# Kernel optimization log

Measured on AMD Instinct MI355X. Metric: run time of the kernel, lower is better.

The kernel has to match this reference:

```python
import jax, jax.numpy as jnp
import numpy as np

D_MODEL = 1024
NUM_HEADS = 16
HEAD_DIM = D_MODEL // NUM_HEADS
HIDDEN = 4096
EPS = 1e-5


def setup_inputs() -> dict:
    key = jax.random.key(0)
    ks = jax.random.split(key, 10)
    s = 0.02
    return {
        "x": jax.random.normal(ks[0], (2, 2048, D_MODEL), dtype=jnp.float32),
        # attention projection weights stored as (in, out): y = x @ W
        "wq": jax.random.normal(ks[1], (D_MODEL, D_MODEL), dtype=jnp.float32) * s,
        "wk": jax.random.normal(ks[2], (D_MODEL, D_MODEL), dtype=jnp.float32) * s,
        "wv": jax.random.normal(ks[3], (D_MODEL, D_MODEL), dtype=jnp.float32) * s,
        "wo": jax.random.normal(ks[4], (D_MODEL, D_MODEL), dtype=jnp.float32) * s,
        # FFN
        "w1": jax.random.normal(ks[5], (D_MODEL, HIDDEN), dtype=jnp.float32) * s,
        "b1": jnp.zeros((HIDDEN,), dtype=jnp.float32),
        "w2": jax.random.normal(ks[6], (HIDDEN, D_MODEL), dtype=jnp.float32) * s,
        "b2": jnp.zeros((D_MODEL,), dtype=jnp.float32),
        # LayerNorms
        "g1": jnp.ones((D_MODEL,), dtype=jnp.float32),
        "be1": jnp.zeros((D_MODEL,), dtype=jnp.float32),
        "g2": jnp.ones((D_MODEL,), dtype=jnp.float32),
        "be2": jnp.zeros((D_MODEL,), dtype=jnp.float32),
    }


def _layernorm(x, g, b):
    mu = jnp.mean(x, axis=-1, keepdims=True)
    var = jnp.mean(jnp.square(x - mu), axis=-1, keepdims=True)
    return (x - mu) * jax.lax.rsqrt(var + EPS) * g + b


def _attention(x, wq, wk, wv, wo):
    B, S, D = x.shape
    q = (x @ wq).reshape(B, S, NUM_HEADS, HEAD_DIM)
    k = (x @ wk).reshape(B, S, NUM_HEADS, HEAD_DIM)
    v = (x @ wv).reshape(B, S, NUM_HEADS, HEAD_DIM)
    scores = jnp.einsum("bqhd,bkhd->bhqk", q, k) / jnp.sqrt(
        jnp.float32(HEAD_DIM)
    )
    causal = jnp.tril(jnp.ones((S, S), dtype=bool))
    scores = jnp.where(causal, scores, -jnp.inf)
    probs = jax.nn.softmax(scores, axis=-1)
    out = jnp.einsum("bhqk,bkhd->bqhd", probs, v).reshape(B, S, D)
    return out @ wo


def _ffn(x, w1, b1, w2, b2):
    return jax.nn.relu(x @ w1 + b1) @ w2 + b2


def reference(x, wq, wk, wv, wo, w1, b1, w2, b2, g1, be1, g2, be2):
    x = x + _attention(_layernorm(x, g1, be1), wq, wk, wv, wo)
    x = x + _ffn(_layernorm(x, g2, be2), w1, b1, w2, b2)
    return x
```

## Files before the change

### kernel.cpp

```cpp
#include <hip/hip_runtime.h>
#include <stdint.h>

typedef unsigned short bf16u;
typedef __attribute__((ext_vector_type(8))) __bf16 bf16x8;
typedef __attribute__((ext_vector_type(4))) float f32x4;
typedef __attribute__((ext_vector_type(4))) unsigned short u16x4;
typedef __attribute__((ext_vector_type(8))) unsigned short u16x8;

typedef __attribute__((address_space(1))) void gvoid_t;
typedef __attribute__((address_space(3))) void lvoid_t;

#define SEQ 2048
#define DM 1024
#define MN22 4194304
#define SCL 0.18033688f

__device__ __forceinline__ bf16u f2bf(float f) {
  union { float f; uint32_t u; } v; v.f = f;
  uint32_t u = v.u + 0x7fffu + ((v.u >> 16) & 1u);
  return (bf16u)(u >> 16);
}

__device__ __forceinline__ bf16u f2bf_hw(float f) {
  union { __bf16 h; bf16u u; } v; v.h = (__bf16)f; return v.u;
}

__device__ __forceinline__ float bf2f(bf16u b) {
  union { uint32_t u; float f; } v; v.u = (uint32_t)b << 16; return v.f;
}

__device__ __forceinline__ float exp2_hw(float x) {
  return __builtin_amdgcn_exp2f(x);
}

__device__ __forceinline__ void async_copy16(const bf16u* g, const bf16u* l) {
  __builtin_amdgcn_global_load_lds((gvoid_t*)(uintptr_t)g,
                                   (lvoid_t*)(uint32_t)(uintptr_t)l,
                                   16, 0, 0);
}

#define VM_WAIT(n) asm volatile("s_waitcnt vmcnt(" #n ")" ::: "memory")
#define LGKM0()    asm volatile("s_waitcnt lgkmcnt(0)" ::: "memory")
#define BARRIER()  asm volatile("s_barrier" ::: "memory")

__global__ __launch_bounds__(256) void ln_kernel(const float* __restrict__ x,
                                                 const float* __restrict__ g,
                                                 const float* __restrict__ be,
                                                 bf16u* __restrict__ out) {
  const int row = blockIdx.x;
  const int t = threadIdx.x;
  const float4 v = ((const float4*)(x + (size_t)row * DM))[t];
  float s  = v.x + v.y + v.z + v.w;
  float ss = v.x * v.x + v.y * v.y + v.z * v.z + v.w * v.w;
#pragma unroll
  for (int m = 1; m < 64; m <<= 1) {
    s  += __shfl_xor(s, m, 64);
    ss += __shfl_xor(ss, m, 64);
  }
  __shared__ float red[2][4];
  const int wv = t >> 6, ln = t & 63;
  if (ln == 0) { red[0][wv] = s; red[1][wv] = ss; }
  __syncthreads();
  s  = red[0][0] + red[0][1] + red[0][2] + red[0][3];
  ss = red[1][0] + red[1][1] + red[1][2] + red[1][3];
  const float mu = s * (1.0f / DM);
  const float var = ss * (1.0f / DM) - mu * mu;
  const float rstd = rsqrtf(var + 1e-5f);
  const float4 gg = ((const float4*)g)[t];
  const float4 bb = ((const float4*)be)[t];
  u16x4 o;
  o[0] = f2bf((v.x - mu) * rstd * gg.x + bb.x);
  o[1] = f2bf((v.y - mu) * rstd * gg.y + bb.y);
  o[2] = f2bf((v.z - mu) * rstd * gg.z + bb.z);
  o[3] = f2bf((v.w - mu) * rstd * gg.w + bb.w);
  *(u16x4*)(out + (size_t)row * DM + t * 4) = o;
}

__global__ __launch_bounds__(256) void prep_kernel(
    const float* __restrict__ x, const float* __restrict__ g,
    const float* __restrict__ be, bf16u* __restrict__ lnout,
    const float* __restrict__ wq, const float* __restrict__ wk,
    const float* __restrict__ wv_, const float* __restrict__ wo,
    bf16u* __restrict__ wqkv_t,
    const float* __restrict__ w1, bf16u* __restrict__ w1_t,
    const float* __restrict__ w2, bf16u* __restrict__ w2_t) {
  const int bid = blockIdx.x;
  const int t = threadIdx.x;
  if (bid < 4096) {
    const int row = bid;
    const float4 v = ((const float4*)(x + (size_t)row * DM))[t];
    float s  = v.x + v.y + v.z + v.w;
    float ss = v.x * v.x + v.y * v.y + v.z * v.z + v.w * v.w;
#pragma unroll
    for (int m = 1; m < 64; m <<= 1) {
      s  += __shfl_xor(s, m, 64);
      ss += __shfl_xor(ss, m, 64);
    }
    __shared__ float red[2][4];
    const int wv = t >> 6, ln = t & 63;
    if (ln == 0) { red[0][wv] = s; red[1][wv] = ss; }
    __syncthreads();
    s  = red[0][0] + red[0][1] + red[0][2] + red[0][3];
    ss = red[1][0] + red[1][1] + red[1][2] + red[1][3];
    const float mu = s * (1.0f / DM);
    const float var = ss * (1.0f / DM) - mu * mu;
    const float rstd = rsqrtf(var + 1e-5f);
    const float4 gg = ((const float4*)g)[t];
    const float4 bb = ((const float4*)be)[t];
    u16x4 o;
    o[0] = f2bf((v.x - mu) * rstd * gg.x + bb.x);
    o[1] = f2bf((v.y - mu) * rstd * gg.y + bb.y);
    o[2] = f2bf((v.z - mu) * rstd * gg.z + bb.z);
    o[3] = f2bf((v.w - mu) * rstd * gg.w + bb.w);
    *(u16x4*)(lnout + (size_t)row * DM + t * 4) = o;
    return;
  }
  __shared__ float tile[32][33];
  const int tx = t & 31, ty = t >> 5;
  const float* in; bf16u* o; int R, C, c0, r0;
  if (bid < 8192) {
    const int idx = bid - 4096;
    const int mat = idx >> 10, rem = idx & 1023;
    const float* srcs[4] = {wq, wk, wv_, wo};
    in = srcs[mat]; o = wqkv_t + (size_t)mat * 1024 * 1024;
    R = 1024; C = 1024;
    c0 = (rem & 31) * 32; r0 = (rem >> 5) * 32;
  } else if (bid < 12288) {
    const int idx = bid - 8192;
    in = w1; o = w1_t; R = 1024; C = 4096;
    c0 = (idx & 127) * 32; r0 = (idx >> 7) * 32;
  } else {
    const int idx = bid - 12288;
    in = w2; o = w2_t; R = 4096; C = 1024;
    c0 = (idx & 31) * 32; r0 = (idx >> 5) * 32;
  }
#pragma unroll
  for (int i = 0; i < 4; ++i)
    tile[ty + i * 8][tx] = in[(size_t)(r0 + ty + i * 8) * C + c0 + tx];
  __syncthreads();
#pragma unroll
  for (int i = 0; i < 4; ++i)
    o[(size_t)(c0 + ty + i * 8) * R + r0 + tx] = f2bf(tile[tx][ty + i * 8]);
}

__global__ __launch_bounds__(256) void reduce3(const bf16u* __restrict__ p01,
                                               const bf16u* __restrict__ p2,
                                               const float* __restrict__ bias,
                                               float* __restrict__ out) {
  const size_t i8 = ((size_t)blockIdx.x * 256 + threadIdx.x) * 8;
  const int col0 = (int)(i8 & 1023);
  const u16x8 a = *(const u16x8*)(p01 + i8);
  const u16x8 b = *(const u16x8*)(p01 + MN22 + i8);
  const u16x8 c = *(const u16x8*)(p2 + i8);
  const float4 o0 = *(const float4*)(out + i8);
  const float4 o1 = *(const float4*)(out + i8 + 4);
  const float4 b0 = *(const float4*)(bias + col0);
  const float4 b1 = *(const float4*)(bias + col0 + 4);
  float r[8];
#pragma unroll
  for (int j = 0; j < 8; ++j) r[j] = bf2f(a[j]) + bf2f(b[j]) + bf2f(c[j]);
  float4 w0, w1;
  w0.x = o0.x + r[0] + b0.x; w0.y = o0.y + r[1] + b0.y;
  w0.z = o0.z + r[2] + b0.z; w0.w = o0.w + r[3] + b0.w;
  w1.x = o1.x + r[4] + b1.x; w1.y = o1.y + r[5] + b1.y;
  w1.z = o1.z + r[6] + b1.z; w1.w = o1.w + r[7] + b1.w;
  *(float4*)(out + i8) = w0;
  *(float4*)(out + i8 + 4) = w1;
}

__global__ __launch_bounds__(256, 2) void gemm256(
    const bf16u* __restrict__ A, const bf16u* __restrict__ Bt,
    int M, int N, int K,
    const float* __restrict__ bias, bf16u* __restrict__ outB,
    bf16u* __restrict__ vt, int mode) {
  __shared__ bf16u sh[2][16384];
  const int t = threadIdx.x;
  const int ln = t & 63;
  const int wv = t >> 6;
  const int col16 = ln & 15, quad = ln >> 4;
  const int wm = wv >> 1, wn = wv & 1;

  const int nsplit = (mode == 6) ? 3 : 1;
  const int nbx = N >> 7;
  const int nwg = nbx * (M >> 7) * nsplit;
  const int cpx = nwg >> 3;
  const int bid = blockIdx.x;
  const int swz = (bid & 7) * cpx + (bid >> 3);
  const int tile = swz / nsplit, split = swz - tile * nsplit;
  const int m0 = (tile / nbx) << 7, n0 = (tile % nbx) << 7;
  const int tsteps = K >> 6;
  const int kbeg = (split * tsteps) / nsplit;
  const int nt = ((split + 1) * tsteps) / nsplit - kbeg;
  const size_t koff = (size_t)kbeg << 6;

  const bf16u* gsrc[4][2];
  int doff[4][2];
#pragma unroll
  for (int j = 0; j < 2; ++j) {
    const int c = t + (j << 8);
    const int lr = c >> 3, slot = (c & 7) ^ (lr & 7);
    const int rq = (lr & 31) + ((lr >> 5) << 6);
    gsrc[0][j] = A  + (size_t)(m0 + rq) * K + koff + slot * 8;
    gsrc[3][j] = A  + (size_t)(m0 + rq + 32) * K + koff + slot * 8;
    gsrc[1][j] = Bt + (size_t)(n0 + rq) * K + koff + slot * 8;
    gsrc[2][j] = Bt + (size_t)(n0 + rq + 32) * K + koff + slot * 8;
    doff[0][j] = c * 8;
    doff[3][j] = 4096 + c * 8;
    doff[1][j] = 8192 + c * 8;
    doff[2][j] = 12288 + c * 8;
  }

  int aoffs[4][2], boffs[4][2];
#pragma unroll
  for (int i = 0; i < 4; ++i)
#pragma unroll
    for (int kc = 0; kc < 2; ++kc) {
      const int ra = wm * 64 + i * 16 + col16;
      const int la = ((ra >> 5) & 1) * 4096 + (((ra & 31) + ((ra >> 6) << 5)) << 6);
      aoffs[i][kc] = la + (((kc << 2) + quad) ^ (ra & 7)) * 8;
      const int rb = wn * 64 + i * 16 + col16;
      const int lb = ((rb >> 5) & 1) * 4096 + (((rb & 31) + ((rb >> 6) << 5)) << 6);
      boffs[i][kc] = 8192 + lb + (((kc << 2) + quad) ^ (rb & 7)) * 8;
    }

  f32x4 acc[4][4] = {};
  bf16x8 Af[2][2], Bf[4][2];

  auto stage = [&](int s, int b) {
#pragma unroll
    for (int j = 0; j < 2; ++j) {
      async_copy16(gsrc[s][j], &sh[b][doff[s][j]]);
      gsrc[s][j] += 64;
    }
  };
  auto readA = [&](int b, int mh) {
#pragma unroll
    for (int i = 0; i < 2; ++i)
#pragma unroll
      for (int kc = 0; kc < 2; ++kc)
        Af[i][kc] = *(const bf16x8*)(&sh[b][aoffs[mh * 2 + i][kc]]);
  };
  auto readB = [&](int b, int nh) {
#pragma unroll
    for (int i = 0; i < 2; ++i)
#pragma unroll
      for (int kc = 0; kc < 2; ++kc)
        Bf[nh * 2 + i][kc] = *(const bf16x8*)(&sh[b][boffs[nh * 2 + i][kc]]);
  };
  auto mfmaQ = [&](int mh, int nh) {
#pragma unroll
    for (int kc = 0; kc < 2; ++kc)
#pragma unroll
      for (int mi = 0; mi < 2; ++mi)
#pragma unroll
        for (int nl = 0; nl < 2; ++nl)
          acc[mh * 2 + mi][nh * 2 + nl] = __builtin_amdgcn_mfma_f32_16x16x32_bf16(
              Af[mi][kc], Bf[nh * 2 + nl][kc], acc[mh * 2 + mi][nh * 2 + nl], 0, 0, 0);
  };

  stage(0, 0); stage(1, 0); stage(2, 0); stage(3, 0);
  VM_WAIT(4);
  BARRIER();

  int bsel = 0;
  for (int kt = 0; kt < nt - 1; ++kt, bsel ^= 1) {
    const int bn = bsel ^ 1;
    readA(bsel, 0); readB(bsel, 0);
    stage(0, bn);
    BARRIER(); LGKM0();
    __builtin_amdgcn_s_setprio(1); mfmaQ(0, 0); __builtin_amdgcn_s_setprio(0);
    VM_WAIT(4); BARRIER();
    readB(bsel, 1);
    stage(1, bn);
    BARRIER(); LGKM0();
    __builtin_amdgcn_s_setprio(1); mfmaQ(0, 1); __builtin_amdgcn_s_setprio(0);
    VM_WAIT(4); BARRIER();
    readA(bsel, 1);
    stage(2, bn);
    BARRIER(); LGKM0();
    __builtin_amdgcn_s_setprio(1); mfmaQ(1, 0); __builtin_amdgcn_s_setprio(0);
    BARRIER();
    stage(3, bn);
    __builtin_amdgcn_s_setprio(1); mfmaQ(1, 1); __builtin_amdgcn_s_setprio(0);
    VM_WAIT(4); BARRIER();
  }
  readA(bsel, 0); readB(bsel, 0);
  BARRIER(); LGKM0();
  __builtin_amdgcn_s_setprio(1); mfmaQ(0, 0); __builtin_amdgcn_s_setprio(0);
  VM_WAIT(2); BARRIER();
  readB(bsel, 1);
  BARRIER(); LGKM0();
  __builtin_amdgcn_s_setprio(1); mfmaQ(0, 1); __builtin_amdgcn_s_setprio(0);
  VM_WAIT(0); BARRIER();
  readA(bsel, 1);
  LGKM0();
  __builtin_amdgcn_s_setprio(1); mfmaQ(1, 0); mfmaQ(1, 1); __builtin_amdgcn_s_setprio(0);

  if (mode == 6) {
    bf16u* pb = (split < 2) ? outB + (size_t)split * MN22 : vt;
#pragma unroll
    for (int mi = 0; mi < 4; ++mi) {
#pragma unroll
      for (int n = 0; n < 4; ++n) {
        const int col = n0 + wn * 64 + n * 16 + col16;
#pragma unroll
        for (int r = 0; r < 4; ++r) {
          const int row = m0 + wm * 64 + mi * 16 + quad * 4 + r;
          pb[(size_t)row * N + col] = f2bf(acc[mi][n][r]);
        }
      }
    }
    return;
  }
  if (mode == 5 && n0 >= 2048) {
#pragma unroll
    for (int mi = 0; mi < 4; ++mi) {
#pragma unroll
      for (int n = 0; n < 4; ++n) {
        const int col = n0 + wn * 64 + n * 16 + col16;
        const int hh = (col - 2048) >> 6, d = (col - 2048) & 63;
        const int row_base = m0 + wm * 64 + mi * 16 + quad * 4;
        const int bb = row_base >> 11, s = row_base & 2047;
        u16x4 o;
#pragma unroll
        for (int r = 0; r < 4; ++r) o[r] = f2bf(acc[mi][n][r]);
        *(u16x4*)(vt + (size_t)((bb * 16 + hh) * 64 + d) * SEQ + s) = o;
      }
    }
    return;
  }
  const float qscale = (mode == 5 && n0 < 1024) ? SCL : 1.0f;
  float bv[4];
  if (mode == 1) {
#pragma unroll
    for (int n = 0; n < 4; ++n) bv[n] = bias[n0 + wn * 64 + n * 16 + col16];
  }
#pragma unroll
  for (int mi = 0; mi < 4; ++mi) {
#pragma unroll
    for (int n = 0; n < 4; ++n) {
      const int col = n0 + wn * 64 + n * 16 + col16;
#pragma unroll
      for (int r = 0; r < 4; ++r) {
        const int row = m0 + wm * 64 + mi * 16 + quad * 4 + r;
        float v = acc[mi][n][r];
        if (mode == 1) v = fmaxf(v + bv[n], 0.0f);
        outB[(size_t)row * N + col] = f2bf(v * qscale);
      }
    }
  }
}

__global__ __launch_bounds__(256, 3) void gemm_bt64(
    const bf16u* __restrict__ A, const bf16u* __restrict__ Bt,
    int M, int N, int K,
    const float* __restrict__ bias, const float* __restrict__ resid,
    bf16u* __restrict__ outB, float* __restrict__ outF, int mode) {
  __shared__ bf16u As0[64 * 64], As1[64 * 64];
  __shared__ bf16u Bs0[128 * 64], Bs1[128 * 64];
  const int t = threadIdx.x;
  const int ln = t & 63;
  const int wv = t >> 6;
  const int col16 = ln & 15, quad = ln >> 4;

  const int nbx = gridDim.x;
  const int nwg = nbx * gridDim.y;
  const int cpx = nwg >> 3;
  const int flat = blockIdx.y * nbx + blockIdx.x;
  const int swz = (flat & 7) * cpx + (flat >> 3);
  const int m0 = (swz / nbx) * 64, n0 = (swz % nbx) * 128;

  const bf16u* gA[2];
  const bf16u* gB[4];
#pragma unroll
  for (int j = 0; j < 2; ++j) {
    const int c = t + 256 * j, row = c >> 3, slot = (c & 7) ^ (row & 7);
    gA[j] = A + (size_t)(m0 + row) * K + slot * 8;
  }
#pragma unroll
  for (int j = 0; j < 4; ++j) {
    const int c = t + 256 * j, row = c >> 3, slot = (c & 7) ^ (row & 7);
    gB[j] = Bt + (size_t)(n0 + row) * K + slot * 8;
  }

  f32x4 acc[4][2] = {};

  auto stage = [&](bf16u* dA, bf16u* dB) {
#pragma unroll
    for (int j = 0; j < 2; ++j) {
      async_copy16(gA[j], dA + (size_t)(t + 256 * j) * 8);
      gA[j] += 64;
    }
#pragma unroll
    for (int j = 0; j < 4; ++j) {
      async_copy16(gB[j], dB + (size_t)(t + 256 * j) * 8);
      gB[j] += 64;
    }
  };
  auto compute = [&](const bf16u* sA, const bf16u* sB) {
    bf16x8 af[4][2], bfv[2][2];
#pragma unroll
    for (int mi = 0; mi < 4; ++mi) {
      const int row = mi * 16 + col16;
#pragma unroll
      for (int kc = 0; kc < 2; ++kc)
        af[mi][kc] = *(const bf16x8*)(sA + row * 64 + (((kc << 2) + quad) ^ (row & 7)) * 8);
    }
#pragma unroll
    for (int ni = 0; ni < 2; ++ni) {
      const int row = wv * 32 + ni * 16 + col16;
#pragma unroll
      for (int kc = 0; kc < 2; ++kc)
        bfv[ni][kc] = *(const bf16x8*)(sB + row * 64 + (((kc << 2) + quad) ^ (row & 7)) * 8);
    }
#pragma unroll
    for (int kc = 0; kc < 2; ++kc)
#pragma unroll
      for (int mi = 0; mi < 4; ++mi)
#pragma unroll
        for (int ni = 0; ni < 2; ++ni)
          acc[mi][ni] = __builtin_amdgcn_mfma_f32_16x16x32_bf16(af[mi][kc], bfv[ni][kc],
                                                                acc[mi][ni], 0, 0, 0);
  };

  const int niter = K >> 6;
  stage(As0, Bs0);
  for (int k = 0; k < niter; k += 2) {
    stage(As1, Bs1);
    VM_WAIT(6);
    BARRIER();
    compute(As0, Bs0);
    BARRIER();
    if (k + 2 < niter) {
      stage(As0, Bs0);
      VM_WAIT(6);
    } else {
      VM_WAIT(0);
    }
    BARRIER();
    compute(As1, Bs1);
    BARRIER();
  }

#pragma unroll
  for (int mi = 0; mi < 4; ++mi) {
#pragma unroll
    for (int ni = 0; ni < 2; ++ni) {
      const int col = n0 + wv * 32 + ni * 16 + col16;
#pragma unroll
      for (int r = 0; r < 4; ++r) {
        const int row = m0 + mi * 16 + quad * 4 + r;
        float v = acc[mi][ni][r];
        if (mode == 1 || mode == 3) v += bias[col];
        if (mode == 1) v = fmaxf(v, 0.0f);
        if (mode >= 2) {
          outF[(size_t)row * N + col] = v + resid[(size_t)row * N + col];
        } else {
          outB[(size_t)row * N + col] = f2bf(v);
        }
      }
    }
  }
}

#define PST 132
__global__ __launch_bounds__(256, 3) void attn_kernel(const bf16u* __restrict__ qkv,
                                                      const bf16u* __restrict__ vt,
                                                      bf16u* __restrict__ out) {
  __shared__ bf16u Ks[128 * 64];
  __shared__ bf16u Vts[2 * 64 * 64];
  __shared__ bf16u pbuf[4][16 * PST];
  __shared__ float lred[4][16];
  const int t = threadIdx.x;
  const int wv = t >> 6, ln = t & 63;
  const int col = ln & 15, quad = ln >> 4;
  const int bh = blockIdx.x, b = bh >> 4, h = bh & 15;
  const int strip = 31 - blockIdx.y;
  const int q0 = strip * 64;
  const int qw = q0 + wv * 16;
  const int qmax = qw + 15;
  const int ntiles = (q0 >> 7) + 1;

  int krow[4], kslot[4], vrow[4], vsub[4], vslot[4];
  const bf16u *kl[4], *vl[4];
#pragma unroll
  for (int j = 0; j < 4; ++j) {
    const int c = t + 256 * j;
    krow[j] = c >> 3; kslot[j] = (c & 7) ^ (krow[j] & 7);
    const int rem = c & 511;
    vsub[j] = c >> 9; vrow[j] = rem >> 3; vslot[j] = (rem & 7) ^ (vrow[j] & 7);
    kl[j] = Ks + (size_t)c * 8;
    vl[j] = Vts + (size_t)c * 8;
  }

  auto stageK = [&](int kb) {
    const int kbase = kb * 128;
#pragma unroll
    for (int j = 0; j < 4; ++j)
      async_copy16(qkv + (size_t)(b * SEQ + kbase + krow[j]) * 3072 + 1024 + h * 64 + kslot[j] * 8, kl[j]);
  };
  auto stageV = [&](int kb) {
    const int kbase = kb * 128;
#pragma unroll
    for (int j = 0; j < 4; ++j)
      async_copy16(vt + (size_t)(bh * 64 + vrow[j]) * SEQ + kbase + vsub[j] * 64 + vslot[j] * 8, vl[j]);
  };

  bf16x8 qf0, qf1;
  {
    const size_t qoff = (size_t)(b * SEQ + qw + col) * 3072 + h * 64 + quad * 8;
    qf0 = *(const bf16x8*)(qkv + qoff);
    qf1 = *(const bf16x8*)(qkv + qoff + 32);
  }
  f32x4 po[4] = {};
  float ll[4] = {};

  stageK(0);
  stageV(0);
  VM_WAIT(4);
  BARRIER();

  for (int kb = 0; kb < ntiles; ++kb) {
    const int kbase = kb * 128;
    if (kb < ntiles - 1) {
      f32x4 sc[8];
      __builtin_amdgcn_s_setprio(1);
#pragma unroll
      for (int n = 0; n < 8; ++n) {
        const int kr = n * 16 + col;
        const bf16x8 k0 = *(const bf16x8*)(Ks + kr * 64 + (quad ^ (kr & 7)) * 8);
        const bf16x8 k1 = *(const bf16x8*)(Ks + kr * 64 + ((4 + quad) ^ (kr & 7)) * 8);
        f32x4 z = {};
        z = __builtin_amdgcn_mfma_f32_16x16x32_bf16(qf0, k0, z, 0, 0, 0);
        sc[n] = __builtin_amdgcn_mfma_f32_16x16x32_bf16(qf1, k1, z, 0, 0, 0);
      }
      __builtin_amdgcn_s_setprio(0);
#pragma unroll
      for (int r = 0; r < 4; ++r) {
#pragma unroll
        for (int n = 0; n < 8; ++n) {
          const float e = exp2_hw(sc[n][r]);
          ll[r] += e;
          pbuf[wv][(quad * 4 + r) * PST + n * 16 + col] = f2bf_hw(e);
        }
      }
    } else {
      f32x4 sc[8];
      bool act[8];
      __builtin_amdgcn_s_setprio(1);
#pragma unroll
      for (int n = 0; n < 8; ++n) {
        act[n] = (kbase + n * 16) <= qmax;
        if (act[n]) {
          const int kr = n * 16 + col;
          const bf16x8 k0 = *(const bf16x8*)(Ks + kr * 64 + (quad ^ (kr & 7)) * 8);
          const bf16x8 k1 = *(const bf16x8*)(Ks + kr * 64 + ((4 + quad) ^ (kr & 7)) * 8);
          f32x4 z = {};
          z = __builtin_amdgcn_mfma_f32_16x16x32_bf16(qf0, k0, z, 0, 0, 0);
          sc[n] = __builtin_amdgcn_mfma_f32_16x16x32_bf16(qf1, k1, z, 0, 0, 0);
        }
      }
      __builtin_amdgcn_s_setprio(0);
#pragma unroll
      for (int r = 0; r < 4; ++r) {
        const int q = qw + quad * 4 + r;
#pragma unroll
        for (int n = 0; n < 8; ++n) {
          float e = 0.0f;
          if (act[n]) {
            float v = sc[n][r];
            v = (kbase + n * 16 + col <= q) ? v : -1e30f;
            e = exp2_hw(v);
          }
          ll[r] += e;
          pbuf[wv][(quad * 4 + r) * PST + n * 16 + col] = f2bf_hw(e);
        }
      }
    }
    LGKM0();
    bf16x8 pa[4];
#pragma unroll
    for (int kc = 0; kc < 4; ++kc)
      pa[kc] = *(const bf16x8*)(&pbuf[wv][col * PST + kc * 32 + quad * 8]);
    VM_WAIT(0);
    BARRIER();
    if (kb + 1 < ntiles) stageK(kb + 1);
    if (kb < ntiles - 1) {
      __builtin_amdgcn_s_setprio(1);
#pragma unroll
      for (int n = 0; n < 4; ++n) {
        const int vr = n * 16 + col;
#pragma unroll
        for (int kc = 0; kc < 4; ++kc) {
          const bf16x8 vfr = *(const bf16x8*)(Vts + (kc >> 1) * 4096 + vr * 64 +
                                              (((kc & 1) * 4 + quad) ^ (vr & 7)) * 8);
          po[n] = __builtin_amdgcn_mfma_f32_16x16x32_bf16(vfr, pa[kc], po[n], 0, 0, 0);
        }
      }
      __builtin_amdgcn_s_setprio(0);
    } else {
      __builtin_amdgcn_s_setprio(1);
#pragma unroll
      for (int n = 0; n < 4; ++n) {
        const int vr = n * 16 + col;
#pragma unroll
        for (int kc = 0; kc < 4; ++kc)
          if (kbase + kc * 32 <= qmax) {
            const bf16x8 vfr = *(const bf16x8*)(Vts + (kc >> 1) * 4096 + vr * 64 +
                                                (((kc & 1) * 4 + quad) ^ (vr & 7)) * 8);
            po[n] = __builtin_amdgcn_mfma_f32_16x16x32_bf16(vfr, pa[kc], po[n], 0, 0, 0);
          }
      }
      __builtin_amdgcn_s_setprio(0);
    }
    if (kb + 1 < ntiles) {
      LGKM0();
      BARRIER();
      stageV(kb + 1);
      VM_WAIT(4);
      BARRIER();
    }
  }

#pragma unroll
  for (int m = 1; m < 16; m <<= 1)
#pragma unroll
    for (int r = 0; r < 4; ++r) ll[r] += __shfl_xor(ll[r], m, 64);
  if (col == 0) {
#pragma unroll
    for (int r = 0; r < 4; ++r) lred[wv][quad * 4 + r] = ll[r];
  }
  LGKM0();
  const float inv = 1.0f / lred[wv][col];
#pragma unroll
  for (int n = 0; n < 4; ++n) {
    u16x4 o;
#pragma unroll
    for (int r = 0; r < 4; ++r) o[r] = f2bf(po[n][r] * inv);
    *(u16x4*)(out + (size_t)(b * SEQ + qw + col) * DM + h * 64 + n * 16 + quad * 4) = o;
  }
}

extern "C" void kernel_launch(void* const* d_in, const int* in_sizes, int n_in,
                              void* d_out, int out_size, void* d_ws, size_t ws_size,
                              hipStream_t stream) {
  const float* x   = (const float*)d_in[0];
  const float* wq  = (const float*)d_in[1];
  const float* wk  = (const float*)d_in[2];
  const float* wvv = (const float*)d_in[3];
  const float* wo  = (const float*)d_in[4];
  const float* w1  = (const float*)d_in[5];
  const float* b1  = (const float*)d_in[6];
  const float* w2  = (const float*)d_in[7];
  const float* b2  = (const float*)d_in[8];
  const float* g1  = (const float*)d_in[9];
  const float* be1 = (const float*)d_in[10];
  const float* g2  = (const float*)d_in[11];
  const float* be2 = (const float*)d_in[12];
  float* out = (float*)d_out;

  char* ws = (char*)d_ws;
  bf16u* wqkv_t = (bf16u*)(ws);
  bf16u* wo_t   = (bf16u*)(ws +  6291456);
  bf16u* w1_t   = (bf16u*)(ws +  8388608);
  bf16u* w2_t   = (bf16u*)(ws + 16777216);
  bf16u* lnbuf  = (bf16u*)(ws + 25165824);
  bf16u* qkv    = (bf16u*)(ws + 33554432);
  bf16u* vtb    = (bf16u*)(ws + 58720256);
  bf16u* h1     = (bf16u*)(ws + 33554432);
  bf16u* attn   = lnbuf;
  bf16u* p01 = (bf16u*)(ws);
  bf16u* p2  = (bf16u*)(ws + 25165824);

  prep_kernel<<<16384, 256, 0, stream>>>(x, g1, be1, lnbuf,
                                         wq, wk, wvv, wo, wqkv_t,
                                         w1, w1_t, w2, w2_t);
  gemm256<<<768, 256, 0, stream>>>(lnbuf, wqkv_t, 4096, 3072, 1024,
                                   nullptr, qkv, vtb, 5);
  attn_kernel<<<dim3(32, 32), 256, 0, stream>>>(qkv, vtb, attn);
  gemm_bt64<<<dim3(8, 64), 256, 0, stream>>>(attn, wo_t, 4096, 1024, 1024,
                                             nullptr, x, nullptr, out, 2);
  ln_kernel<<<4096, 256, 0, stream>>>(out, g2, be2, lnbuf);
  gemm256<<<1024, 256, 0, stream>>>(lnbuf, w1_t, 4096, 4096, 1024,
                                    b1, h1, nullptr, 1);
  gemm256<<<768, 256, 0, stream>>>(h1, w2_t, 4096, 1024, 4096,
                                   nullptr, p01, p2, 6);
  reduce3<<<2048, 256, 0, stream>>>(p01, p2, b2, out);
}
```

Before: 318.4 us.

## Use 512-thread blocks in gemm256 with 2x4 wave grid and restructured pipeline

Doubles the threads per 128x128 GEMM tile from 4 to 8 waves, giving each wave a 64x32 sub-tile and halving its accumulator and register footprint. Each thread now issues one async copy per stage, and the per-iteration pipeline is reorganised into two halves with the tail folded into the main loop. The intent is more waves in flight to hide memory and LDS latency. The cost is more barrier traffic per tile and more LDS fragment reads across waves, since B reuse per wave drops.

```diff
diff --git a/kernel.cpp b/kernel.cpp
--- a/kernel.cpp
+++ b/kernel.cpp
@@ -168,7 +168,7 @@
   *(float4*)(out + i8 + 4) = w1;
 }
 
-__global__ __launch_bounds__(256, 2) void gemm256(
+__global__ __launch_bounds__(512, 4) void gemm256(
     const bf16u* __restrict__ A, const bf16u* __restrict__ Bt,
     int M, int N, int K,
     const float* __restrict__ bias, bf16u* __restrict__ outB,
@@ -178,7 +178,7 @@
   const int ln = t & 63;
   const int wv = t >> 6;
   const int col16 = ln & 15, quad = ln >> 4;
-  const int wm = wv >> 1, wn = wv & 1;
+  const int wm = wv >> 2, wn = wv & 3;
 
   const int nsplit = (mode == 6) ? 3 : 1;
   const int nbx = N >> 7;
@@ -193,116 +193,103 @@
   const int nt = ((split + 1) * tsteps) / nsplit - kbeg;
   const size_t koff = (size_t)kbeg << 6;
 
-  const bf16u* gsrc[4][2];
-  int doff[4][2];
-#pragma unroll
-  for (int j = 0; j < 2; ++j) {
-    const int c = t + (j << 8);
-    const int lr = c >> 3, slot = (c & 7) ^ (lr & 7);
-    const int rq = (lr & 31) + ((lr >> 5) << 6);
-    gsrc[0][j] = A  + (size_t)(m0 + rq) * K + koff + slot * 8;
-    gsrc[3][j] = A  + (size_t)(m0 + rq + 32) * K + koff + slot * 8;
-    gsrc[1][j] = Bt + (size_t)(n0 + rq) * K + koff + slot * 8;
-    gsrc[2][j] = Bt + (size_t)(n0 + rq + 32) * K + koff + slot * 8;
-    doff[0][j] = c * 8;
-    doff[3][j] = 4096 + c * 8;
-    doff[1][j] = 8192 + c * 8;
-    doff[2][j] = 12288 + c * 8;
-  }
-
-  int aoffs[4][2], boffs[4][2];
-#pragma unroll
-  for (int i = 0; i < 4; ++i)
+  const int lr = t >> 3, slot = (t & 7) ^ (lr & 7);
+  const int rq = (lr & 31) + ((lr >> 5) << 6);
+  const bf16u* gsrc[4];
+  gsrc[0] = Bt + (size_t)(n0 + rq) * K + koff + slot * 8;
+  gsrc[1] = Bt + (size_t)(n0 + rq + 32) * K + koff + slot * 8;
+  gsrc[2] = A  + (size_t)(m0 + rq) * K + koff + slot * 8;
+  gsrc[3] = A  + (size_t)(m0 + rq + 32) * K + koff + slot * 8;
+  int doff[4];
+  doff[0] = 8192  + t * 8;
+  doff[1] = 12288 + t * 8;
+  doff[2] = 0     + t * 8;
+  doff[3] = 4096  + t * 8;
+
+  int aoffs[2][2][2], boffs[2][2];
+#pragma unroll
+  for (int h = 0; h < 2; ++h)
+#pragma unroll
+    for (int i = 0; i < 2; ++i)
+#pragma unroll
+      for (int kc = 0; kc < 2; ++kc) {
+        const int ra = wm * 64 + h * 32 + i * 16 + col16;
+        const int la = ((ra >> 5) & 1) * 4096 + (((ra & 31) + ((ra >> 6) << 5)) << 6);
+        aoffs[h][i][kc] = la + (((kc << 2) + quad) ^ (ra & 7)) * 8;
+      }
+#pragma unroll
+  for (int i = 0; i < 2; ++i)
 #pragma unroll
     for (int kc = 0; kc < 2; ++kc) {
-      const int ra = wm * 64 + i * 16 + col16;
-      const int la = ((ra >> 5) & 1) * 4096 + (((ra & 31) + ((ra >> 6) << 5)) << 6);
-      aoffs[i][kc] = la + (((kc << 2) + quad) ^ (ra & 7)) * 8;
-      const int rb = wn * 64 + i * 16 + col16;
+      const int rb = wn * 32 + i * 16 + col16;
       const int lb = ((rb >> 5) & 1) * 4096 + (((rb & 31) + ((rb >> 6) << 5)) << 6);
       boffs[i][kc] = 8192 + lb + (((kc << 2) + quad) ^ (rb & 7)) * 8;
     }
 
-  f32x4 acc[4][4] = {};
-  bf16x8 Af[2][2], Bf[4][2];
+  f32x4 acc[4][2] = {};
+  bf16x8 Af[2][2], Bf[2][2];
 
   auto stage = [&](int s, int b) {
-#pragma unroll
-    for (int j = 0; j < 2; ++j) {
-      async_copy16(gsrc[s][j], &sh[b][doff[s][j]]);
-      gsrc[s][j] += 64;
-    }
-  };
-  auto readA = [&](int b, int mh) {
+    async_copy16(gsrc[s], &sh[b][doff[s]]);
+    gsrc[s] += 64;
+  };
+  auto readA = [&](int b, int h) {
 #pragma unroll
     for (int i = 0; i < 2; ++i)
 #pragma unroll
       for (int kc = 0; kc < 2; ++kc)
-        Af[i][kc] = *(const bf16x8*)(&sh[b][aoffs[mh * 2 + i][kc]]);
-  };
-  auto readB = [&](int b, int nh) {
+        Af[i][kc] = *(const bf16x8*)(&sh[b][aoffs[h][i][kc]]);
+  };
+  auto readB = [&](int b) {
 #pragma unroll
     for (int i = 0; i < 2; ++i)
 #pragma unroll
       for (int kc = 0; kc < 2; ++kc)
-        Bf[nh * 2 + i][kc] = *(const bf16x8*)(&sh[b][boffs[nh * 2 + i][kc]]);
-  };
-  auto mfmaQ = [&](int mh, int nh) {
+        Bf[i][kc] = *(const bf16x8*)(&sh[b][boffs[i][kc]]);
+  };
+  auto mfmaH = [&](int h) {
 #pragma unroll
     for (int kc = 0; kc < 2; ++kc)
 #pragma unroll
       for (int mi = 0; mi < 2; ++mi)
 #pragma unroll
-        for (int nl = 0; nl < 2; ++nl)
-          acc[mh * 2 + mi][nh * 2 + nl] = __builtin_amdgcn_mfma_f32_16x16x32_bf16(
-              Af[mi][kc], Bf[nh * 2 + nl][kc], acc[mh * 2 + mi][nh * 2 + nl], 0, 0, 0);
+        for (int ni = 0; ni < 2; ++ni)
+          acc[h * 2 + mi][ni] = __builtin_amdgcn_mfma_f32_16x16x32_bf16(
+              Af[mi][kc], Bf[ni][kc], acc[h * 2 + mi][ni], 0, 0, 0);
   };
 
   stage(0, 0); stage(1, 0); stage(2, 0); stage(3, 0);
-  VM_WAIT(4);
+  VM_WAIT(1);
   BARRIER();
 
   int bsel = 0;
-  for (int kt = 0; kt < nt - 1; ++kt, bsel ^= 1) {
+  for (int kt = 0; kt < nt; ++kt, bsel ^= 1) {
     const int bn = bsel ^ 1;
-    readA(bsel, 0); readB(bsel, 0);
-    stage(0, bn);
+    const bool more = (kt + 1 < nt);
+    readB(bsel); readA(bsel, 0);
+    if (more) stage(0, bn);
     BARRIER(); LGKM0();
-    __builtin_amdgcn_s_setprio(1); mfmaQ(0, 0); __builtin_amdgcn_s_setprio(0);
-    VM_WAIT(4); BARRIER();
-    readB(bsel, 1);
-    stage(1, bn);
+    __builtin_amdgcn_s_setprio(1); mfmaH(0); __builtin_amdgcn_s_setprio(0);
+    if (more) { VM_WAIT(1); } else { VM_WAIT(0); }
+    BARRIER();
+    readA(bsel, 1);
+    if (more) { stage(1, bn); stage(2, bn); }
     BARRIER(); LGKM0();
-    __builtin_amdgcn_s_setprio(1); mfmaQ(0, 1); __builtin_amdgcn_s_setprio(0);
-    VM_WAIT(4); BARRIER();
-    readA(bsel, 1);
-    stage(2, bn);
-    BARRIER(); LGKM0();
-    __builtin_amdgcn_s_setprio(1); mfmaQ(1, 0); __builtin_amdgcn_s_setprio(0);
+    __builtin_amdgcn_s_setprio(1); mfmaH(1); __builtin_amdgcn_s_setprio(0);
+    if (more) {
+      stage(3, bn);
+      VM_WAIT(1);
+    }
     BARRIER();
-    stage(3, bn);
-    __builtin_amdgcn_s_setprio(1); mfmaQ(1, 1); __builtin_amdgcn_s_setprio(0);
-    VM_WAIT(4); BARRIER();
-  }
-  readA(bsel, 0); readB(bsel, 0);
-  BARRIER(); LGKM0();
-  __builtin_amdgcn_s_setprio(1); mfmaQ(0, 0); __builtin_amdgcn_s_setprio(0);
-  VM_WAIT(2); BARRIER();
-  readB(bsel, 1);
-  BARRIER(); LGKM0();
-  __builtin_amdgcn_s_setprio(1); mfmaQ(0, 1); __builtin_amdgcn_s_setprio(0);
-  VM_WAIT(0); BARRIER();
-  readA(bsel, 1);
-  LGKM0();
-  __builtin_amdgcn_s_setprio(1); mfmaQ(1, 0); mfmaQ(1, 1); __builtin_amdgcn_s_setprio(0);
+  }
 
   if (mode == 6) {
     bf16u* pb = (split < 2) ? outB + (size_t)split * MN22 : vt;
 #pragma unroll
     for (int mi = 0; mi < 4; ++mi) {
 #pragma unroll
-      for (int n = 0; n < 4; ++n) {
-        const int col = n0 + wn * 64 + n * 16 + col16;
+      for (int n = 0; n < 2; ++n) {
+        const int col = n0 + wn * 32 + n * 16 + col16;
 #pragma unroll
         for (int r = 0; r < 4; ++r) {
           const int row = m0 + wm * 64 + mi * 16 + quad * 4 + r;
@@ -316,8 +303,8 @@
 #pragma unroll
     for (int mi = 0; mi < 4; ++mi) {
 #pragma unroll
-      for (int n = 0; n < 4; ++n) {
-        const int col = n0 + wn * 64 + n * 16 + col16;
+      for (int n = 0; n < 2; ++n) {
+        const int col = n0 + wn * 32 + n * 16 + col16;
         const int hh = (col - 2048) >> 6, d = (col - 2048) & 63;
         const int row_base = m0 + wm * 64 + mi * 16 + quad * 4;
         const int bb = row_base >> 11, s = row_base & 2047;
@@ -330,16 +317,16 @@
     return;
   }
   const float qscale = (mode == 5 && n0 < 1024) ? SCL : 1.0f;
-  float bv[4];
+  float bv[2];
   if (mode == 1) {
 #pragma unroll
-    for (int n = 0; n < 4; ++n) bv[n] = bias[n0 + wn * 64 + n * 16 + col16];
+    for (int n = 0; n < 2; ++n) bv[n] = bias[n0 + wn * 32 + n * 16 + col16];
   }
 #pragma unroll
   for (int mi = 0; mi < 4; ++mi) {
 #pragma unroll
-    for (int n = 0; n < 4; ++n) {
-      const int col = n0 + wn * 64 + n * 16 + col16;
+    for (int n = 0; n < 2; ++n) {
+      const int col = n0 + wn * 32 + n * 16 + col16;
 #pragma unroll
       for (int r = 0; r < 4; ++r) {
         const int row = m0 + wm * 64 + mi * 16 + quad * 4 + r;
@@ -675,15 +662,15 @@
   prep_kernel<<<16384, 256, 0, stream>>>(x, g1, be1, lnbuf,
                                          wq, wk, wvv, wo, wqkv_t,
                                          w1, w1_t, w2, w2_t);
-  gemm256<<<768, 256, 0, stream>>>(lnbuf, wqkv_t, 4096, 3072, 1024,
+  gemm256<<<768, 512, 0, stream>>>(lnbuf, wqkv_t, 4096, 3072, 1024,
                                    nullptr, qkv, vtb, 5);
   attn_kernel<<<dim3(32, 32), 256, 0, stream>>>(qkv, vtb, attn);
   gemm_bt64<<<dim3(8, 64), 256, 0, stream>>>(attn, wo_t, 4096, 1024, 1024,
                                              nullptr, x, nullptr, out, 2);
   ln_kernel<<<4096, 256, 0, stream>>>(out, g2, be2, lnbuf);
-  gemm256<<<1024, 256, 0, stream>>>(lnbuf, w1_t, 4096, 4096, 1024,
+  gemm256<<<1024, 512, 0, stream>>>(lnbuf, w1_t, 4096, 4096, 1024,
                                     b1, h1, nullptr, 1);
-  gemm256<<<768, 256, 0, stream>>>(h1, w2_t, 4096, 1024, 4096,
+  gemm256<<<768, 512, 0, stream>>>(h1, w2_t, 4096, 1024, 4096,
                                    nullptr, p01, p2, 6);
   reduce3<<<2048, 256, 0, stream>>>(p01, p2, b2, out);
 }
```

Result: slower. 336.2 us (+5.6%).

## Drop split-K for FFN down-projection and fuse bias/residual into GEMM epilogue

Applied to the files above, without the earlier changes.

The second FFN GEMM no longer splits K three ways with bf16 partial buffers and a separate reduce kernel. It now runs 256 full-K 128x128 tiles and adds bias and residual directly into the fp32 output in the epilogue. This removes the partial-sum writes and reads and one kernel launch, and keeps full fp32 accumulation. The cost is that only 256 workgroups are launched, which may underfill the GPU's compute units, and the epilogue does scattered read-modify-write stores.

```diff
diff --git a/kernel.cpp b/kernel.cpp
--- a/kernel.cpp
+++ b/kernel.cpp
@@ -143,36 +143,11 @@
     o[(size_t)(c0 + ty + i * 8) * R + r0 + tx] = f2bf(tile[tx][ty + i * 8]);
 }
 
-__global__ __launch_bounds__(256) void reduce3(const bf16u* __restrict__ p01,
-                                               const bf16u* __restrict__ p2,
-                                               const float* __restrict__ bias,
-                                               float* __restrict__ out) {
-  const size_t i8 = ((size_t)blockIdx.x * 256 + threadIdx.x) * 8;
-  const int col0 = (int)(i8 & 1023);
-  const u16x8 a = *(const u16x8*)(p01 + i8);
-  const u16x8 b = *(const u16x8*)(p01 + MN22 + i8);
-  const u16x8 c = *(const u16x8*)(p2 + i8);
-  const float4 o0 = *(const float4*)(out + i8);
-  const float4 o1 = *(const float4*)(out + i8 + 4);
-  const float4 b0 = *(const float4*)(bias + col0);
-  const float4 b1 = *(const float4*)(bias + col0 + 4);
-  float r[8];
-#pragma unroll
-  for (int j = 0; j < 8; ++j) r[j] = bf2f(a[j]) + bf2f(b[j]) + bf2f(c[j]);
-  float4 w0, w1;
-  w0.x = o0.x + r[0] + b0.x; w0.y = o0.y + r[1] + b0.y;
-  w0.z = o0.z + r[2] + b0.z; w0.w = o0.w + r[3] + b0.w;
-  w1.x = o1.x + r[4] + b1.x; w1.y = o1.y + r[5] + b1.y;
-  w1.z = o1.z + r[6] + b1.z; w1.w = o1.w + r[7] + b1.w;
-  *(float4*)(out + i8) = w0;
-  *(float4*)(out + i8 + 4) = w1;
-}
-
 __global__ __launch_bounds__(256, 2) void gemm256(
     const bf16u* __restrict__ A, const bf16u* __restrict__ Bt,
     int M, int N, int K,
     const float* __restrict__ bias, bf16u* __restrict__ outB,
-    bf16u* __restrict__ vt, int mode) {
+    bf16u* __restrict__ vt, float* __restrict__ outF, int mode) {
   __shared__ bf16u sh[2][16384];
   const int t = threadIdx.x;
   const int ln = t & 63;
@@ -180,18 +155,13 @@
   const int col16 = ln & 15, quad = ln >> 4;
   const int wm = wv >> 1, wn = wv & 1;
 
-  const int nsplit = (mode == 6) ? 3 : 1;
   const int nbx = N >> 7;
-  const int nwg = nbx * (M >> 7) * nsplit;
+  const int nwg = nbx * (M >> 7);
   const int cpx = nwg >> 3;
   const int bid = blockIdx.x;
   const int swz = (bid & 7) * cpx + (bid >> 3);
-  const int tile = swz / nsplit, split = swz - tile * nsplit;
-  const int m0 = (tile / nbx) << 7, n0 = (tile % nbx) << 7;
-  const int tsteps = K >> 6;
-  const int kbeg = (split * tsteps) / nsplit;
-  const int nt = ((split + 1) * tsteps) / nsplit - kbeg;
-  const size_t koff = (size_t)kbeg << 6;
+  const int m0 = (swz / nbx) << 7, n0 = (swz % nbx) << 7;
+  const int nt = K >> 6;
 
   const bf16u* gsrc[4][2];
   int doff[4][2];
@@ -200,10 +170,10 @@
     const int c = t + (j << 8);
     const int lr = c >> 3, slot = (c & 7) ^ (lr & 7);
     const int rq = (lr & 31) + ((lr >> 5) << 6);
-    gsrc[0][j] = A  + (size_t)(m0 + rq) * K + koff + slot * 8;
-    gsrc[3][j] = A  + (size_t)(m0 + rq + 32) * K + koff + slot * 8;
-    gsrc[1][j] = Bt + (size_t)(n0 + rq) * K + koff + slot * 8;
-    gsrc[2][j] = Bt + (size_t)(n0 + rq + 32) * K + koff + slot * 8;
+    gsrc[0][j] = A  + (size_t)(m0 + rq) * K + slot * 8;
+    gsrc[3][j] = A  + (size_t)(m0 + rq + 32) * K + slot * 8;
+    gsrc[1][j] = Bt + (size_t)(n0 + rq) * K + slot * 8;
+    gsrc[2][j] = Bt + (size_t)(n0 + rq + 32) * K + slot * 8;
     doff[0][j] = c * 8;
     doff[3][j] = 4096 + c * 8;
     doff[1][j] = 8192 + c * 8;
@@ -296,8 +266,10 @@
   LGKM0();
   __builtin_amdgcn_s_setprio(1); mfmaQ(1, 0); mfmaQ(1, 1); __builtin_amdgcn_s_setprio(0);
 
-  if (mode == 6) {
-    bf16u* pb = (split < 2) ? outB + (size_t)split * MN22 : vt;
+  if (mode == 7) {
+    float bv[4];
+#pragma unroll
+    for (int n = 0; n < 4; ++n) bv[n] = bias[n0 + wn * 64 + n * 16 + col16];
 #pragma unroll
     for (int mi = 0; mi < 4; ++mi) {
 #pragma unroll
@@ -306,7 +278,8 @@
 #pragma unroll
         for (int r = 0; r < 4; ++r) {
           const int row = m0 + wm * 64 + mi * 16 + quad * 4 + r;
-          pb[(size_t)row * N + col] = f2bf(acc[mi][n][r]);
+          const size_t idx = (size_t)row * N + col;
+          outF[idx] = outF[idx] + acc[mi][n][r] + bv[n];
         }
       }
     }
@@ -669,21 +642,18 @@
   bf16u* vtb    = (bf16u*)(ws + 58720256);
   bf16u* h1     = (bf16u*)(ws + 33554432);
   bf16u* attn   = lnbuf;
-  bf16u* p01 = (bf16u*)(ws);
-  bf16u* p2  = (bf16u*)(ws + 25165824);
 
   prep_kernel<<<16384, 256, 0, stream>>>(x, g1, be1, lnbuf,
                                          wq, wk, wvv, wo, wqkv_t,
                                          w1, w1_t, w2, w2_t);
   gemm256<<<768, 256, 0, stream>>>(lnbuf, wqkv_t, 4096, 3072, 1024,
-                                   nullptr, qkv, vtb, 5);
+                                   nullptr, qkv, vtb, nullptr, 5);
   attn_kernel<<<dim3(32, 32), 256, 0, stream>>>(qkv, vtb, attn);
   gemm_bt64<<<dim3(8, 64), 256, 0, stream>>>(attn, wo_t, 4096, 1024, 1024,
                                              nullptr, x, nullptr, out, 2);
   ln_kernel<<<4096, 256, 0, stream>>>(out, g2, be2, lnbuf);
   gemm256<<<1024, 256, 0, stream>>>(lnbuf, w1_t, 4096, 4096, 1024,
-                                    b1, h1, nullptr, 1);
-  gemm256<<<768, 256, 0, stream>>>(h1, w2_t, 4096, 1024, 4096,
-                                   nullptr, p01, p2, 6);
-  reduce3<<<2048, 256, 0, stream>>>(p01, p2, b2, out);
-}
+                                    b1, h1, nullptr, nullptr, 1);
+  gemm256<<<256, 256, 0, stream>>>(h1, w2_t, 4096, 1024, 4096,
+                                   b2, nullptr, nullptr, out, 7);
+}
```

New measurement: 324.2 us. Within noise of the previous version (+1.8%).
